# Kernel optimization log

Hardware: AMD Instinct MI355X
Metric: run time of the kernel (lower is better)

Reference implementation:

```python
import jax, jax.numpy as jnp
import numpy as np

NEG_INF = -1.0e9  # value used by masked_fill in the original

def setup_inputs() -> dict:
    key = jax.random.key(0)
    kq, kk, kv, km = jax.random.split(key, 4)
    B, H, S, D = 2, 16, 2048, 64
    query = jax.random.normal(kq, (B, H, S, D), dtype=jnp.float32)
    key_t = jax.random.normal(kk, (B, H, S, D), dtype=jnp.float32)
    value = jax.random.normal(kv, (B, H, S, D), dtype=jnp.float32)
    mask = jax.random.randint(km, (1, 1, S, S), 0, 2, dtype=jnp.int32)
    return {"query": query, "key": key_t, "value": value, "mask": mask}

def reference(query, key, value, mask):
    d_k = query.shape[-1]
    # scores: [B,H,Sq,Sk]
    scores = jnp.einsum("bhqd,bhkd->bhqk", query, key) / jnp.sqrt(jnp.float32(d_k))
    scores = jnp.where(mask == 0, jnp.float32(NEG_INF), scores)
    attn = jax.nn.softmax(scores, axis=-1)
    out = jnp.einsum("bhqk,bhkd->bhqd", attn, value)
    return (out, attn)
```

## Files before the change

kernel.cpp:

```cpp
#include <hip/hip_runtime.h>


#define S_LEN 2048
#define D_DIM 64
#define BH_N  32
#define NELEM (BH_N*S_LEN*D_DIM)

typedef __bf16 bf16;
typedef bf16 bf16x4 __attribute__((ext_vector_type(4)));
typedef bf16 bf16x8 __attribute__((ext_vector_type(8)));
typedef float f32x4 __attribute__((ext_vector_type(4)));

__device__ __attribute__((aligned(16))) bf16 g_Qb[NELEM];
__device__ __attribute__((aligned(16))) bf16 g_Kb[NELEM];
__device__ __attribute__((aligned(16))) bf16 g_VT[NELEM];
__device__ unsigned long long g_bits[S_LEN*S_LEN/64];

__device__ __forceinline__ void gload16(const bf16* g, bf16* l){
  __builtin_amdgcn_global_load_lds(
      (const __attribute__((address_space(1))) void*)g,
      (__attribute__((address_space(3))) void*)l, 16, 0, 0);
}

__global__ void cvt_qk_kernel(const float* __restrict__ Qs, const float* __restrict__ Ks){
  int i = blockIdx.x*256 + threadIdx.x;
  float4 q = reinterpret_cast<const float4*>(Qs)[i];
  float4 k = reinterpret_cast<const float4*>(Ks)[i];
  bf16x4 oq = {(bf16)q.x,(bf16)q.y,(bf16)q.z,(bf16)q.w};
  bf16x4 ok = {(bf16)k.x,(bf16)k.y,(bf16)k.z,(bf16)k.w};
  ((bf16x4*)g_Qb)[i] = oq;
  ((bf16x4*)g_Kb)[i] = ok;
}

__global__ void transpose_v_kernel(const float* __restrict__ V){
  __shared__ float sv[64][65];
  int bh = blockIdx.x >> 5;
  int k0 = (blockIdx.x & 31) << 6;
  const float* src = V + ((size_t)bh*S_LEN + k0)*D_DIM;
  #pragma unroll
  for (int i=0;i<16;i++){
    int e = threadIdx.x + i*256;
    sv[e>>6][e&63] = src[e];
  }
  __syncthreads();
  bf16* dst = g_VT + (size_t)bh*D_DIM*S_LEN + k0;
  #pragma unroll
  for (int i=0;i<16;i++){
    int e = threadIdx.x + i*256;
    int d = e>>6, k = e&63;
    dst[(size_t)d*S_LEN + k] = (bf16)sv[k][d];
  }
}

__global__ void build_bits_kernel(const int* __restrict__ mask){
  int gid = blockIdx.x*256 + threadIdx.x;
  unsigned long long b = __ballot(mask[gid] != 0);
  if ((threadIdx.x & 63) == 0) g_bits[gid >> 6] = b;
}

__global__ __launch_bounds__(256, 4)
void attn_main_kernel(float* __restrict__ out, float* __restrict__ attn){
  __shared__ __attribute__((aligned(16))) bf16 s_pool[5*64*64];
  bf16* const kd0 = s_pool;
  bf16* const kd1 = s_pool + 4096;
  bf16* const vd0 = s_pool + 8192;
  bf16* const vd1 = s_pool + 12288;
  bf16* const sp  = s_pool + 16384;

  const int tid  = threadIdx.x;
  const int wave = tid >> 6, lane = tid & 63;
  const int quad = lane >> 4, l16 = lane & 15;
  const int bh = blockIdx.x >> 5, qb = blockIdx.x & 31;
  const int q0 = qb << 6, m0 = wave << 4;

  const bf16* __restrict__ Qh  = g_Qb + ((size_t)bh*S_LEN + q0)*D_DIM;
  const bf16* __restrict__ Kh  = g_Kb + (size_t)bh*S_LEN*D_DIM;
  const bf16* __restrict__ VTh = g_VT + (size_t)bh*D_DIM*S_LEN;
  float* __restrict__ outh  = out  + ((size_t)bh*S_LEN + q0)*D_DIM;
  float* __restrict__ attnh = attn + (size_t)bh*S_LEN*S_LEN + (size_t)q0*S_LEN;

  const int s0 = tid, s1 = tid + 256;
  const int r0 = s0>>3, b0 = (s0&7)^(r0&7);
  const int r1 = s1>>3, b1 = (s1&7)^(r1&7);
  const int    gk0 = r0*D_DIM + b0*8, gk1 = r1*D_DIM + b1*8;
  const size_t gv0 = (size_t)r0*S_LEN + b0*8, gv1 = (size_t)r1*S_LEN + b1*8;
  const int lb0 = (wave<<6)*8, lb1 = (256 + (wave<<6))*8;

  gload16(Qh  + gk0, sp  + lb0);  gload16(Qh  + gk1, sp  + lb1);
  gload16(Kh  + gk0, kd0 + lb0);  gload16(Kh  + gk1, kd0 + lb1);
  gload16(VTh + gv0, vd0 + lb0);  gload16(VTh + gv1, vd0 + lb1);
  __syncthreads();

  const int arow = m0 + l16;
  const bf16x8 aq0 = *(const bf16x8*)&sp[(arow<<6) + ((quad     ^ (arow&7))<<3)];
  const bf16x8 aq1 = *(const bf16x8*)&sp[(arow<<6) + (((quad+4) ^ (arow&7))<<3)];

  float lp[4] = {0.f,0.f,0.f,0.f};
  f32x4 oacc[4];
  #pragma unroll
  for (int n=0;n<4;n++) oacc[n] = (f32x4){0.f,0.f,0.f,0.f};

  const int mrow = q0 + m0 + quad*4;
  const size_t mbase = (size_t)mrow * 32;

  for (int kt=0; kt<32; ++kt){
    bf16* const kcur = (kt&1) ? kd1 : kd0;
    bf16* const vcur = (kt&1) ? vd1 : vd0;
    if (kt < 31){
      bf16* const knxt = (kt&1) ? kd0 : kd1;
      bf16* const vnxt = (kt&1) ? vd0 : vd1;
      const bf16* Ks = Kh  + (size_t)((kt+1)<<6)*D_DIM;
      const bf16* Vs = VTh + ((kt+1)<<6);
      gload16(Ks+gk0, knxt+lb0);  gload16(Ks+gk1, knxt+lb1);
      gload16(Vs+gv0, vnxt+lb0);  gload16(Vs+gv1, vnxt+lb1);
    }
    unsigned long long wr_[4];
    #pragma unroll
    for (int r=0;r<4;r++) wr_[r] = g_bits[mbase + r*32 + kt];

    #pragma unroll
    for (int n=0;n<4;n++){
      const int krow = n*16 + l16;
      const bf16x8 bk0 = *(const bf16x8*)&kcur[(krow<<6) + ((quad     ^ (krow&7))<<3)];
      const bf16x8 bk1 = *(const bf16x8*)&kcur[(krow<<6) + (((quad+4) ^ (krow&7))<<3)];
      __builtin_amdgcn_s_setprio(1);
      f32x4 c = (f32x4){0.f,0.f,0.f,0.f};
      c = __builtin_amdgcn_mfma_f32_16x16x32_bf16(aq0, bk0, c, 0,0,0);
      c = __builtin_amdgcn_mfma_f32_16x16x32_bf16(aq1, bk1, c, 0,0,0);
      __builtin_amdgcn_s_setprio(0);
      const int shift = n*16 + l16;
      #pragma unroll
      for (int r=0;r<4;r++){
        float p = ((wr_[r] >> shift) & 1ull) ? __expf(c[r]*0.125f) : 0.f;
        lp[r] += p;
        const int prow = m0 + quad*4 + r;
        sp[(prow<<6) + (((shift>>3)^(prow&7))<<3) + (shift&7)] = (bf16)p;
      }
    }

    __builtin_amdgcn_s_setprio(1);
    #pragma unroll
    for (int s=0;s<2;s++){
      const bf16x8 pa = *(const bf16x8*)&sp[(arow<<6) + (((s*4+quad)^(arow&7))<<3)];
      #pragma unroll
      for (int n=0;n<4;n++){
        const int vrow = n*16 + l16;
        const bf16x8 vb = *(const bf16x8*)&vcur[(vrow<<6) + (((s*4+quad)^(vrow&7))<<3)];
        oacc[n] = __builtin_amdgcn_mfma_f32_16x16x32_bf16(pa, vb, oacc[n], 0,0,0);
      }
    }
    __builtin_amdgcn_s_setprio(0);
    __syncthreads();
  }

  gload16(Kh+gk0, kd0+lb0);  gload16(Kh+gk1, kd0+lb1);

  #pragma unroll
  for (int r=0;r<4;r++){
    float v = lp[r];
    #pragma unroll
    for (int off=1; off<16; off<<=1) v += __shfl_xor(v, off);
    lp[r] = 1.0f / v;
  }

  #pragma unroll
  for (int n=0;n<4;n++){
    #pragma unroll
    for (int r=0;r<4;r++)
      outh[(size_t)(m0 + quad*4 + r)*D_DIM + n*16 + l16] = oacc[n][r] * lp[r];
  }

  __syncthreads();

  for (int kt=0; kt<32; ++kt){
    bf16* const kcur = (kt&1) ? kd1 : kd0;
    if (kt < 31){
      bf16* const knxt = (kt&1) ? kd0 : kd1;
      const bf16* Ks = Kh + (size_t)((kt+1)<<6)*D_DIM;
      gload16(Ks+gk0, knxt+lb0);  gload16(Ks+gk1, knxt+lb1);
    }
    unsigned long long wr_[4];
    #pragma unroll
    for (int r=0;r<4;r++) wr_[r] = g_bits[mbase + r*32 + kt];

    #pragma unroll
    for (int n=0;n<4;n++){
      const int krow = n*16 + l16;
      const bf16x8 bk0 = *(const bf16x8*)&kcur[(krow<<6) + ((quad     ^ (krow&7))<<3)];
      const bf16x8 bk1 = *(const bf16x8*)&kcur[(krow<<6) + (((quad+4) ^ (krow&7))<<3)];
      __builtin_amdgcn_s_setprio(1);
      f32x4 c = (f32x4){0.f,0.f,0.f,0.f};
      c = __builtin_amdgcn_mfma_f32_16x16x32_bf16(aq0, bk0, c, 0,0,0);
      c = __builtin_amdgcn_mfma_f32_16x16x32_bf16(aq1, bk1, c, 0,0,0);
      __builtin_amdgcn_s_setprio(0);
      const int shift = n*16 + l16;
      #pragma unroll
      for (int r=0;r<4;r++){
        float a = ((wr_[r] >> shift) & 1ull) ? __expf(c[r]*0.125f)*lp[r] : 0.f;
        attnh[(size_t)(m0 + quad*4 + r)*S_LEN + (kt<<6) + shift] = a;
      }
    }
    __syncthreads();
  }
}

extern "C" void kernel_launch(void* const* d_in, const int* in_sizes, int n_in,
                              void* d_out, int out_size, void* d_ws, size_t ws_size,
                              hipStream_t stream){
  (void)in_sizes; (void)n_in; (void)d_ws; (void)ws_size; (void)out_size;
  const float* Q    = (const float*)d_in[0];
  const float* K    = (const float*)d_in[1];
  const float* V    = (const float*)d_in[2];
  const int*   mask = (const int*)d_in[3];
  float* out  = (float*)d_out;
  float* attn = out + (size_t)NELEM;

  cvt_qk_kernel     <<<NELEM/4/256,        256, 0, stream>>>(Q, K);
  transpose_v_kernel<<<BH_N*(S_LEN/64),    256, 0, stream>>>(V);
  build_bits_kernel <<<S_LEN*S_LEN/256,    256, 0, stream>>>(mask);
  attn_main_kernel  <<<BH_N*(S_LEN/64),    256, 0, stream>>>(out, attn);
}
```

Before: 708.8 us.

## Load K/V fragments directly from global memory, drop LDS staging and barriers

Removes the double-buffered LDS staging of K and V along with the per-tile __syncthreads. Each wave now loads its MFMA operand fragments straight from global memory (relying on L1/L2 reuse across the 4 waves), and only the P tile stays in a padded LDS array. It also remaps block indices so that consecutive blocks land on different bh heads, which may spread work across XCDs or caches. In exchange, each wave issues redundant global loads and has no software prefetch, so load latency is exposed unless occupancy hides it. P is written and read by the same wave, so the barrier removal looks safe.

Measured after the change: 938.8 us. 32.4% more time.

```diff
diff --git a/kernel.cpp b/kernel.cpp
--- a/kernel.cpp
+++ b/kernel.cpp
@@ -15,12 +15,6 @@
 __device__ __attribute__((aligned(16))) bf16 g_Kb[NELEM];
 __device__ __attribute__((aligned(16))) bf16 g_VT[NELEM];
 __device__ unsigned long long g_bits[S_LEN*S_LEN/64];
-
-__device__ __forceinline__ void gload16(const bf16* g, bf16* l){
-  __builtin_amdgcn_global_load_lds(
-      (const __attribute__((address_space(1))) void*)g,
-      (__attribute__((address_space(3))) void*)l, 16, 0, 0);
-}
 
 __global__ void cvt_qk_kernel(const float* __restrict__ Qs, const float* __restrict__ Ks){
   int i = blockIdx.x*256 + threadIdx.x;
@@ -60,17 +54,14 @@
 
 __global__ __launch_bounds__(256, 4)
 void attn_main_kernel(float* __restrict__ out, float* __restrict__ attn){
-  __shared__ __attribute__((aligned(16))) bf16 s_pool[5*64*64];
-  bf16* const kd0 = s_pool;
-  bf16* const kd1 = s_pool + 4096;
-  bf16* const vd0 = s_pool + 8192;
-  bf16* const vd1 = s_pool + 12288;
-  bf16* const sp  = s_pool + 16384;
+  __shared__ __attribute__((aligned(16))) bf16 sP[64][72];
 
   const int tid  = threadIdx.x;
   const int wave = tid >> 6, lane = tid & 63;
   const int quad = lane >> 4, l16 = lane & 15;
-  const int bh = blockIdx.x >> 5, qb = blockIdx.x & 31;
+
+  const int logical = ((blockIdx.x & 7) << 7) + (blockIdx.x >> 3);
+  const int bh = logical >> 5, qb = logical & 31;
   const int q0 = qb << 6, m0 = wave << 4;
 
   const bf16* __restrict__ Qh  = g_Qb + ((size_t)bh*S_LEN + q0)*D_DIM;
@@ -79,21 +70,9 @@
   float* __restrict__ outh  = out  + ((size_t)bh*S_LEN + q0)*D_DIM;
   float* __restrict__ attnh = attn + (size_t)bh*S_LEN*S_LEN + (size_t)q0*S_LEN;
 
-  const int s0 = tid, s1 = tid + 256;
-  const int r0 = s0>>3, b0 = (s0&7)^(r0&7);
-  const int r1 = s1>>3, b1 = (s1&7)^(r1&7);
-  const int    gk0 = r0*D_DIM + b0*8, gk1 = r1*D_DIM + b1*8;
-  const size_t gv0 = (size_t)r0*S_LEN + b0*8, gv1 = (size_t)r1*S_LEN + b1*8;
-  const int lb0 = (wave<<6)*8, lb1 = (256 + (wave<<6))*8;
-
-  gload16(Qh  + gk0, sp  + lb0);  gload16(Qh  + gk1, sp  + lb1);
-  gload16(Kh  + gk0, kd0 + lb0);  gload16(Kh  + gk1, kd0 + lb1);
-  gload16(VTh + gv0, vd0 + lb0);  gload16(VTh + gv1, vd0 + lb1);
-  __syncthreads();
-
   const int arow = m0 + l16;
-  const bf16x8 aq0 = *(const bf16x8*)&sp[(arow<<6) + ((quad     ^ (arow&7))<<3)];
-  const bf16x8 aq1 = *(const bf16x8*)&sp[(arow<<6) + (((quad+4) ^ (arow&7))<<3)];
+  const bf16x8 aq0 = *(const bf16x8*)&Qh[arow*D_DIM + quad*8];
+  const bf16x8 aq1 = *(const bf16x8*)&Qh[arow*D_DIM + 32 + quad*8];
 
   float lp[4] = {0.f,0.f,0.f,0.f};
   f32x4 oacc[4];
@@ -104,56 +83,49 @@
   const size_t mbase = (size_t)mrow * 32;
 
   for (int kt=0; kt<32; ++kt){
-    bf16* const kcur = (kt&1) ? kd1 : kd0;
-    bf16* const vcur = (kt&1) ? vd1 : vd0;
-    if (kt < 31){
-      bf16* const knxt = (kt&1) ? kd0 : kd1;
-      bf16* const vnxt = (kt&1) ? vd0 : vd1;
-      const bf16* Ks = Kh  + (size_t)((kt+1)<<6)*D_DIM;
-      const bf16* Vs = VTh + ((kt+1)<<6);
-      gload16(Ks+gk0, knxt+lb0);  gload16(Ks+gk1, knxt+lb1);
-      gload16(Vs+gv0, vnxt+lb0);  gload16(Vs+gv1, vnxt+lb1);
+    const bf16* __restrict__ Ks = Kh  + (size_t)(kt<<6)*D_DIM;
+    const bf16* __restrict__ Vs = VTh + (kt<<6);
+
+    bf16x8 bk[4][2];
+    #pragma unroll
+    for (int n=0;n<4;n++){
+      const bf16* p = Ks + (n*16 + l16)*D_DIM + quad*8;
+      bk[n][0] = *(const bf16x8*)p;
+      bk[n][1] = *(const bf16x8*)(p + 32);
     }
+
     unsigned long long wr_[4];
     #pragma unroll
     for (int r=0;r<4;r++) wr_[r] = g_bits[mbase + r*32 + kt];
 
     #pragma unroll
     for (int n=0;n<4;n++){
-      const int krow = n*16 + l16;
-      const bf16x8 bk0 = *(const bf16x8*)&kcur[(krow<<6) + ((quad     ^ (krow&7))<<3)];
-      const bf16x8 bk1 = *(const bf16x8*)&kcur[(krow<<6) + (((quad+4) ^ (krow&7))<<3)];
       __builtin_amdgcn_s_setprio(1);
       f32x4 c = (f32x4){0.f,0.f,0.f,0.f};
-      c = __builtin_amdgcn_mfma_f32_16x16x32_bf16(aq0, bk0, c, 0,0,0);
-      c = __builtin_amdgcn_mfma_f32_16x16x32_bf16(aq1, bk1, c, 0,0,0);
+      c = __builtin_amdgcn_mfma_f32_16x16x32_bf16(aq0, bk[n][0], c, 0,0,0);
+      c = __builtin_amdgcn_mfma_f32_16x16x32_bf16(aq1, bk[n][1], c, 0,0,0);
       __builtin_amdgcn_s_setprio(0);
       const int shift = n*16 + l16;
       #pragma unroll
       for (int r=0;r<4;r++){
         float p = ((wr_[r] >> shift) & 1ull) ? __expf(c[r]*0.125f) : 0.f;
         lp[r] += p;
-        const int prow = m0 + quad*4 + r;
-        sp[(prow<<6) + (((shift>>3)^(prow&7))<<3) + (shift&7)] = (bf16)p;
+        sP[m0 + quad*4 + r][shift] = (bf16)p;
       }
     }
 
-    __builtin_amdgcn_s_setprio(1);
     #pragma unroll
     for (int s=0;s<2;s++){
-      const bf16x8 pa = *(const bf16x8*)&sp[(arow<<6) + (((s*4+quad)^(arow&7))<<3)];
+      const bf16x8 pa = *(const bf16x8*)&sP[m0 + l16][s*32 + quad*8];
+      __builtin_amdgcn_s_setprio(1);
       #pragma unroll
       for (int n=0;n<4;n++){
-        const int vrow = n*16 + l16;
-        const bf16x8 vb = *(const bf16x8*)&vcur[(vrow<<6) + (((s*4+quad)^(vrow&7))<<3)];
+        const bf16x8 vb = *(const bf16x8*)&Vs[(size_t)(n*16 + l16)*S_LEN + s*32 + quad*8];
         oacc[n] = __builtin_amdgcn_mfma_f32_16x16x32_bf16(pa, vb, oacc[n], 0,0,0);
       }
+      __builtin_amdgcn_s_setprio(0);
     }
-    __builtin_amdgcn_s_setprio(0);
-    __syncthreads();
   }
-
-  gload16(Kh+gk0, kd0+lb0);  gload16(Kh+gk1, kd0+lb1);
 
   #pragma unroll
   for (int r=0;r<4;r++){
@@ -170,28 +142,27 @@
       outh[(size_t)(m0 + quad*4 + r)*D_DIM + n*16 + l16] = oacc[n][r] * lp[r];
   }
 
-  __syncthreads();
+  for (int kt=0; kt<32; ++kt){
+    const bf16* __restrict__ Ks = Kh + (size_t)(kt<<6)*D_DIM;
 
-  for (int kt=0; kt<32; ++kt){
-    bf16* const kcur = (kt&1) ? kd1 : kd0;
-    if (kt < 31){
-      bf16* const knxt = (kt&1) ? kd0 : kd1;
-      const bf16* Ks = Kh + (size_t)((kt+1)<<6)*D_DIM;
-      gload16(Ks+gk0, knxt+lb0);  gload16(Ks+gk1, knxt+lb1);
+    bf16x8 bk[4][2];
+    #pragma unroll
+    for (int n=0;n<4;n++){
+      const bf16* p = Ks + (n*16 + l16)*D_DIM + quad*8;
+      bk[n][0] = *(const bf16x8*)p;
+      bk[n][1] = *(const bf16x8*)(p + 32);
     }
+
     unsigned long long wr_[4];
     #pragma unroll
     for (int r=0;r<4;r++) wr_[r] = g_bits[mbase + r*32 + kt];
 
     #pragma unroll
     for (int n=0;n<4;n++){
-      const int krow = n*16 + l16;
-      const bf16x8 bk0 = *(const bf16x8*)&kcur[(krow<<6) + ((quad     ^ (krow&7))<<3)];
-      const bf16x8 bk1 = *(const bf16x8*)&kcur[(krow<<6) + (((quad+4) ^ (krow&7))<<3)];
       __builtin_amdgcn_s_setprio(1);
       f32x4 c = (f32x4){0.f,0.f,0.f,0.f};
-      c = __builtin_amdgcn_mfma_f32_16x16x32_bf16(aq0, bk0, c, 0,0,0);
-      c = __builtin_amdgcn_mfma_f32_16x16x32_bf16(aq1, bk1, c, 0,0,0);
+      c = __builtin_amdgcn_mfma_f32_16x16x32_bf16(aq0, bk[n][0], c, 0,0,0);
+      c = __builtin_amdgcn_mfma_f32_16x16x32_bf16(aq1, bk[n][1], c, 0,0,0);
       __builtin_amdgcn_s_setprio(0);
       const int shift = n*16 + l16;
       #pragma unroll
@@ -200,7 +171,6 @@
         attnh[(size_t)(m0 + quad*4 + r)*S_LEN + (kt<<6) + shift] = a;
       }
     }
-    __syncthreads();
   }
 }
 
```
